# Kernel tuning notes

Hardware: AMD Instinct MI355X
Metric: run time of the kernel (lower is better)

Reference implementation:

```python
import jax, jax.numpy as jnp
import numpy as np

B, T, D, U = 128, 256, 256, 1024


def setup_inputs() -> dict:
    key = jax.random.key(0)
    ks = jax.random.split(key, 5)
    features = jax.random.normal(ks[0], (B, T, D), dtype=jnp.float32)
    # irregular positive time deltas in (0, 1)
    time_steps = jax.random.uniform(ks[1], (B, T), dtype=jnp.float32)
    scale_x = 1.0 / np.sqrt(D)
    scale_h = 1.0 / np.sqrt(U)
    Wx = jax.random.normal(ks[2], (D, 2 * U), dtype=jnp.float32) * scale_x
    Wh = jax.random.normal(ks[3], (U, 2 * U), dtype=jnp.float32) * scale_h
    b = jnp.zeros((2 * U,), dtype=jnp.float32)
    w_tau = jax.random.uniform(ks[4], (U,), dtype=jnp.float32)
    h0 = jnp.zeros((B, U), dtype=jnp.float32)
    return {"features": features, "time_steps": time_steps, "Wx": Wx,
            "Wh": Wh, "b": b, "w_tau": w_tau, "h0": h0}


def reference(features, time_steps, Wx, Wh, b, w_tau, h0):
    """IrregularRNN with exact closed-form LTC cell, return_sequences=True.

    Per step: f = sigmoid(pre_f), A = tanh(pre_a),
              h' = (h - A) * exp(-dt * (softplus(w_tau) + f)) + A
    """
    tau = jax.nn.softplus(w_tau)  # [U]

    def step(h, xt):
        x_t, dt_t = xt                      # [B,D], [B]
        pre = x_t @ Wx + h @ Wh + b         # [B,2U]
        f = jax.nn.sigmoid(pre[:, :U])
        a = jnp.tanh(pre[:, U:])
        decay = jnp.exp(-dt_t[:, None] * (tau + f))
        h_new = (h - a) * decay + a
        return h_new, h_new

    xs = (jnp.swapaxes(features, 0, 1), jnp.swapaxes(time_steps, 0, 1))
    _, ys = jax.lax.scan(step, h0, xs)      # ys: [T,B,U]
    return jnp.swapaxes(ys, 0, 1)           # [B,T,U]
```

## Files before the change

### kernel.cpp

```cpp
#include <hip/hip_runtime.h>

typedef _Float16 v8h  __attribute__((ext_vector_type(8)));
typedef _Float16 v4h  __attribute__((ext_vector_type(4)));
typedef float    v4f  __attribute__((ext_vector_type(4)));
typedef unsigned int u32x4 __attribute__((ext_vector_type(4)));

#define BATCH   128
#define TSTEPS  256
#define DFEAT   256
#define UDIM    1024
#define NCOL    2048
#define ASTRIDE 1288


__global__ __launch_bounds__(1024)
void ltc_rnn_kernel(const float* __restrict__ features,
                    const float* __restrict__ tsteps,
                    const float* __restrict__ Wx,
                    const float* __restrict__ Wh,
                    const float* __restrict__ bias,
                    const float* __restrict__ wtau,
                    const float* __restrict__ h0,
                    float* __restrict__ out,
                    unsigned* __restrict__ flags,
                    _Float16* __restrict__ hbufs)
{
  __shared__ _Float16 Alds[16 * ASTRIDE];
  __shared__ float    Plds[16 * 64 * 4];
  __shared__ _Float16 Hout[16][32];
  __shared__ float    dtlds[2][16];

  const int tid  = threadIdx.x;
  const int w    = tid >> 6;
  const int lane = tid & 63;
  const int n    = lane & 15;
  const int q    = lane >> 4;
  const int cg   = w & 3;
  const int ks   = w >> 2;
  const int g    = blockIdx.x & 7;
  const int cb   = blockIdx.x >> 3;
  const int u0   = cb * 32;

  const int gcol = (n < 8) ? (u0 + cg * 8 + n) : (UDIM + u0 + cg * 8 + (n - 8));
  v8h bfr[10];
  #pragma unroll
  for (int c = 0; c < 10; ++c) {
    #pragma unroll
    for (int j = 0; j < 8; ++j) {
      const int k = ks * 320 + c * 32 + q * 8 + j;
      const float wv = (k < DFEAT) ? Wx[(size_t)k * NCOL + gcol]
                                   : Wh[(size_t)(k - DFEAT) * NCOL + gcol];
      bfr[c][j] = (_Float16)wv;
    }
  }

  const float bias_own = bias[gcol];
  const int   u_lane   = u0 + cg * 8 + (n & 7);
  const float tau      = logf(1.0f + __expf(wtau[u_lane]));

  float h_reg[4];
  #pragma unroll
  for (int i = 0; i < 4; ++i)
    h_reg[i] = h0[(size_t)(g * 16 + q * 4 + i) * UDIM + u_lane];

  if (tid < 16) dtlds[0][tid] = tsteps[(size_t)(g * 16 + tid) * TSTEPS + 0];
  {
    const int r = tid >> 6, k4 = tid & 63;
    v4f x4 = *(const v4f*)(features + (size_t)(g * 16 + r) * (TSTEPS * DFEAT) + k4 * 4);
    v4h xh = {(_Float16)x4.x, (_Float16)x4.y, (_Float16)x4.z, (_Float16)x4.w};
    *(v4h*)&Alds[r * ASTRIDE + k4 * 4] = xh;
    #pragma unroll
    for (int jj = 0; jj < 4; ++jj) {
      const int c = tid + jj * 1024, hr = c >> 8, hk4 = c & 255;
      v4f h4 = *(const v4f*)(h0 + (size_t)(g * 16 + hr) * UDIM + hk4 * 4);
      v4h hh = {(_Float16)h4.x, (_Float16)h4.y, (_Float16)h4.z, (_Float16)h4.w};
      *(v4h*)&Alds[hr * ASTRIDE + DFEAT + hk4 * 4] = hh;
    }
  }
  __syncthreads();

  for (int t = 0; t < TSTEPS; ++t) {
    const bool more = (t + 1 < TSTEPS);
    _Float16* hdst = hbufs + ((t + 1) & 1) * (BATCH * UDIM);

    {
      v4f acc = {0.f, 0.f, 0.f, 0.f};
      const _Float16* abase = &Alds[n * ASTRIDE + ks * 320 + q * 8];
      #pragma unroll
      for (int c = 0; c < 10; ++c) {
        v8h a = *(const v8h*)(abase + c * 32);
        acc = __builtin_amdgcn_mfma_f32_16x16x32_f16(a, bfr[c], acc, 0, 0, 0);
      }
      *(v4f*)&Plds[(w * 64 + lane) * 4] = acc;
    }
    __syncthreads();

    float outv[4];
    if (w < 4) {
      v4f p = *(v4f*)&Plds[((0 * 4 + w) * 64 + lane) * 4];
      #pragma unroll
      for (int s = 1; s < 4; ++s) {
        v4f ps = *(v4f*)&Plds[((s * 4 + w) * 64 + lane) * 4];
        p.x += ps.x; p.y += ps.y; p.z += ps.z; p.w += ps.w;
      }
      float pf[4], pa[4];
      #pragma unroll
      for (int i = 0; i < 4; ++i) {
        const float v = p[i] + bias_own;
        const float o = __shfl_xor(v, 8);
        pf[i] = v; pa[i] = o;
      }
      if (n < 8) {
        #pragma unroll
        for (int i = 0; i < 4; ++i) {
          const int   row_l = q * 4 + i;
          const float dt    = dtlds[t & 1][row_l];
          const float f     = 1.0f / (1.0f + __expf(-pf[i]));
          const float av    = 2.0f / (1.0f + __expf(-2.0f * pa[i])) - 1.0f;
          const float decay = __expf(-dt * (tau + f));
          const float hn    = (h_reg[i] - av) * decay + av;
          h_reg[i] = hn;
          outv[i]  = hn;
          Hout[row_l][w * 8 + n] = (_Float16)hn;
        }
      }
    }
    __syncthreads();

    if (w == 0 && more) {
      const int row = lane >> 2, c8 = lane & 3;
      v8h hv = *(v8h*)&Hout[row][c8 * 8];
      _Float16* dp = hdst + (size_t)(g * 16 + row) * UDIM + u0 + c8 * 8;
      asm volatile("global_store_dwordx4 %0, %1, off sc0 sc1\n\t"
                   "s_waitcnt vmcnt(0)"
                   :: "v"(dp), "v"(__builtin_bit_cast(u32x4, hv)) : "memory");
      if (lane == 0) {
        unsigned tg = (unsigned)(t + 1);
        asm volatile("global_store_dword %0, %1, off sc0 sc1"
                     :: "v"(&flags[g * 64 + cb]), "v"(tg) : "memory");
      }
    }

    if (w < 4 && n < 8) {
      #pragma unroll
      for (int i = 0; i < 4; ++i) {
        const int row = g * 16 + q * 4 + i;
        out[(size_t)row * (TSTEPS * UDIM) + (size_t)t * UDIM + u_lane] = outv[i];
      }
    }
    if (more) {
      if (tid < 16) dtlds[(t + 1) & 1][tid] = tsteps[(size_t)(g * 16 + tid) * TSTEPS + t + 1];
      const int r = tid >> 6, k4 = tid & 63;
      v4f x4 = *(const v4f*)(features + (size_t)(g * 16 + r) * (TSTEPS * DFEAT)
                             + (size_t)(t + 1) * DFEAT + k4 * 4);
      v4h xh = {(_Float16)x4.x, (_Float16)x4.y, (_Float16)x4.z, (_Float16)x4.w};
      *(v4h*)&Alds[r * ASTRIDE + k4 * 4] = xh;
    }

    if (w == 0 && more) {
      const unsigned* fp = &flags[g * 64 + (lane & 31)];
      const unsigned  tg = (unsigned)t;
      for (;;) {
        unsigned v;
        asm volatile("global_load_dword %0, %1, off sc0 sc1\n\t"
                     "s_waitcnt vmcnt(0)"
                     : "=v"(v) : "v"(fp) : "memory");
        if (__ballot(v <= tg) == 0ull) break;
      }
    }
    __syncthreads();

    if (more) {
      const _Float16* hsrc = hbufs + ((t + 1) & 1) * (BATCH * UDIM);
      const int c0 = tid, c1 = tid + 1024;
      const _Float16* p0 = hsrc + (size_t)(g * 16 + (c0 >> 7)) * UDIM + (c0 & 127) * 8;
      const _Float16* p1 = hsrc + (size_t)(g * 16 + (c1 >> 7)) * UDIM + (c1 & 127) * 8;
      u32x4 r0, r1;
      asm volatile("global_load_dwordx4 %0, %2, off sc0 sc1\n\t"
                   "global_load_dwordx4 %1, %3, off sc0 sc1\n\t"
                   "s_waitcnt vmcnt(0)"
                   : "=v"(r0), "=v"(r1) : "v"(p0), "v"(p1) : "memory");
      *(v8h*)&Alds[(c0 >> 7) * ASTRIDE + DFEAT + (c0 & 127) * 8] = __builtin_bit_cast(v8h, r0);
      *(v8h*)&Alds[(c1 >> 7) * ASTRIDE + DFEAT + (c1 & 127) * 8] = __builtin_bit_cast(v8h, r1);
      __syncthreads();
    }
  }
}

extern "C" void kernel_launch(void* const* d_in, const int* in_sizes, int n_in,
                              void* d_out, int out_size, void* d_ws, size_t ws_size,
                              hipStream_t stream) {
  const float* features = (const float*)d_in[0];
  const float* tsamp    = (const float*)d_in[1];
  const float* Wx       = (const float*)d_in[2];
  const float* Wh       = (const float*)d_in[3];
  const float* bias     = (const float*)d_in[4];
  const float* wtau     = (const float*)d_in[5];
  const float* h0       = (const float*)d_in[6];
  float*     out    = (float*)d_out;
  unsigned*  flags  = (unsigned*)d_ws;
  _Float16*  hbufs  = (_Float16*)((char*)d_ws + 4096);

  hipMemsetAsync(d_ws, 0, 4096, stream);
  hipLaunchKernelGGL(ltc_rnn_kernel, dim3(256), dim3(1024), 0, stream,
                     features, tsamp, Wx, Wh, bias, wtau, h0, out, flags, hbufs);
}
```

Measured before the change: 1.029 ms.

## Interleave two batch groups per block to hide cross-block flag waits

Each block now handles two batch groups (gA and gB) using the same column slice, so the grid shrinks from 256 to 128 blocks. The two groups' recurrence phases alternate, so while one group waits for the other blocks' hidden-state flags, the other group's step can run. This is meant to hide global synchronization latency behind independent work. The MFMA chain is also split across two accumulators to cut dependency stalls. In exchange the block needs twice the LDS for the A tiles, and each block now serializes two groups' work, so per-step compute on each CU doubles.

```diff
diff --git a/kernel.cpp b/kernel.cpp
--- a/kernel.cpp
+++ b/kernel.cpp
@@ -13,7 +13,7 @@
 #define ASTRIDE 1288
 
 
-__global__ __launch_bounds__(1024)
+__global__ __launch_bounds__(1024, 4)
 void ltc_rnn_kernel(const float* __restrict__ features,
                     const float* __restrict__ tsteps,
                     const float* __restrict__ Wx,
@@ -25,10 +25,12 @@
                     unsigned* __restrict__ flags,
                     _Float16* __restrict__ hbufs)
 {
-  __shared__ _Float16 Alds[16 * ASTRIDE];
+  __shared__ _Float16 AldsA[16 * ASTRIDE];
+  __shared__ _Float16 AldsB[16 * ASTRIDE];
   __shared__ float    Plds[16 * 64 * 4];
   __shared__ _Float16 Hout[16][32];
-  __shared__ float    dtlds[2][16];
+  __shared__ float    dtA[2][16];
+  __shared__ float    dtB[2][16];
 
   const int tid  = threadIdx.x;
   const int w    = tid >> 6;
@@ -37,9 +39,11 @@
   const int q    = lane >> 4;
   const int cg   = w & 3;
   const int ks   = w >> 2;
-  const int g    = blockIdx.x & 7;
-  const int cb   = blockIdx.x >> 3;
+  const int gp   = blockIdx.x & 3;
+  const int cb   = blockIdx.x >> 2;
   const int u0   = cb * 32;
+  const int gA   = gp;
+  const int gB   = gp + 4;
 
   const int gcol = (n < 8) ? (u0 + cg * 8 + n) : (UDIM + u0 + cg * 8 + (n - 8));
   v8h bfr[10];
@@ -58,108 +62,36 @@
   const int   u_lane   = u0 + cg * 8 + (n & 7);
   const float tau      = logf(1.0f + __expf(wtau[u_lane]));
 
-  float h_reg[4];
+  float h_regA[4], h_regB[4];
   #pragma unroll
-  for (int i = 0; i < 4; ++i)
-    h_reg[i] = h0[(size_t)(g * 16 + q * 4 + i) * UDIM + u_lane];
-
-  if (tid < 16) dtlds[0][tid] = tsteps[(size_t)(g * 16 + tid) * TSTEPS + 0];
-  {
+  for (int i = 0; i < 4; ++i) {
+    h_regA[i] = h0[(size_t)(gA * 16 + q * 4 + i) * UDIM + u_lane];
+    h_regB[i] = h0[(size_t)(gB * 16 + q * 4 + i) * UDIM + u_lane];
+  }
+
+  auto prestage = [&](const int g, _Float16* __restrict__ Ald, float (&dtl)[2][16]) {
+    if (tid < 16) dtl[0][tid] = tsteps[(size_t)(g * 16 + tid) * TSTEPS + 0];
     const int r = tid >> 6, k4 = tid & 63;
     v4f x4 = *(const v4f*)(features + (size_t)(g * 16 + r) * (TSTEPS * DFEAT) + k4 * 4);
     v4h xh = {(_Float16)x4.x, (_Float16)x4.y, (_Float16)x4.z, (_Float16)x4.w};
-    *(v4h*)&Alds[r * ASTRIDE + k4 * 4] = xh;
+    *(v4h*)&Ald[r * ASTRIDE + k4 * 4] = xh;
     #pragma unroll
     for (int jj = 0; jj < 4; ++jj) {
       const int c = tid + jj * 1024, hr = c >> 8, hk4 = c & 255;
       v4f h4 = *(const v4f*)(h0 + (size_t)(g * 16 + hr) * UDIM + hk4 * 4);
       v4h hh = {(_Float16)h4.x, (_Float16)h4.y, (_Float16)h4.z, (_Float16)h4.w};
-      *(v4h*)&Alds[hr * ASTRIDE + DFEAT + hk4 * 4] = hh;
-    }
-  }
+      *(v4h*)&Ald[hr * ASTRIDE + DFEAT + hk4 * 4] = hh;
+    }
+  };
+  prestage(gA, AldsA, dtA);
+  prestage(gB, AldsB, dtB);
   __syncthreads();
 
-  for (int t = 0; t < TSTEPS; ++t) {
-    const bool more = (t + 1 < TSTEPS);
-    _Float16* hdst = hbufs + ((t + 1) & 1) * (BATCH * UDIM);
-
-    {
-      v4f acc = {0.f, 0.f, 0.f, 0.f};
-      const _Float16* abase = &Alds[n * ASTRIDE + ks * 320 + q * 8];
-      #pragma unroll
-      for (int c = 0; c < 10; ++c) {
-        v8h a = *(const v8h*)(abase + c * 32);
-        acc = __builtin_amdgcn_mfma_f32_16x16x32_f16(a, bfr[c], acc, 0, 0, 0);
-      }
-      *(v4f*)&Plds[(w * 64 + lane) * 4] = acc;
-    }
-    __syncthreads();
-
-    float outv[4];
-    if (w < 4) {
-      v4f p = *(v4f*)&Plds[((0 * 4 + w) * 64 + lane) * 4];
-      #pragma unroll
-      for (int s = 1; s < 4; ++s) {
-        v4f ps = *(v4f*)&Plds[((s * 4 + w) * 64 + lane) * 4];
-        p.x += ps.x; p.y += ps.y; p.z += ps.z; p.w += ps.w;
-      }
-      float pf[4], pa[4];
-      #pragma unroll
-      for (int i = 0; i < 4; ++i) {
-        const float v = p[i] + bias_own;
-        const float o = __shfl_xor(v, 8);
-        pf[i] = v; pa[i] = o;
-      }
-      if (n < 8) {
-        #pragma unroll
-        for (int i = 0; i < 4; ++i) {
-          const int   row_l = q * 4 + i;
-          const float dt    = dtlds[t & 1][row_l];
-          const float f     = 1.0f / (1.0f + __expf(-pf[i]));
-          const float av    = 2.0f / (1.0f + __expf(-2.0f * pa[i])) - 1.0f;
-          const float decay = __expf(-dt * (tau + f));
-          const float hn    = (h_reg[i] - av) * decay + av;
-          h_reg[i] = hn;
-          outv[i]  = hn;
-          Hout[row_l][w * 8 + n] = (_Float16)hn;
-        }
-      }
-    }
-    __syncthreads();
-
-    if (w == 0 && more) {
-      const int row = lane >> 2, c8 = lane & 3;
-      v8h hv = *(v8h*)&Hout[row][c8 * 8];
-      _Float16* dp = hdst + (size_t)(g * 16 + row) * UDIM + u0 + c8 * 8;
-      asm volatile("global_store_dwordx4 %0, %1, off sc0 sc1\n\t"
-                   "s_waitcnt vmcnt(0)"
-                   :: "v"(dp), "v"(__builtin_bit_cast(u32x4, hv)) : "memory");
-      if (lane == 0) {
-        unsigned tg = (unsigned)(t + 1);
-        asm volatile("global_store_dword %0, %1, off sc0 sc1"
-                     :: "v"(&flags[g * 64 + cb]), "v"(tg) : "memory");
-      }
-    }
-
-    if (w < 4 && n < 8) {
-      #pragma unroll
-      for (int i = 0; i < 4; ++i) {
-        const int row = g * 16 + q * 4 + i;
-        out[(size_t)row * (TSTEPS * UDIM) + (size_t)t * UDIM + u_lane] = outv[i];
-      }
-    }
-    if (more) {
-      if (tid < 16) dtlds[(t + 1) & 1][tid] = tsteps[(size_t)(g * 16 + tid) * TSTEPS + t + 1];
-      const int r = tid >> 6, k4 = tid & 63;
-      v4f x4 = *(const v4f*)(features + (size_t)(g * 16 + r) * (TSTEPS * DFEAT)
-                             + (size_t)(t + 1) * DFEAT + k4 * 4);
-      v4h xh = {(_Float16)x4.x, (_Float16)x4.y, (_Float16)x4.z, (_Float16)x4.w};
-      *(v4h*)&Alds[r * ASTRIDE + k4 * 4] = xh;
-    }
-
-    if (w == 0 && more) {
+  auto phase = [&](const int g, _Float16* __restrict__ Ald,
+                   float (&hreg)[4], float (&dtl)[2][16], const int t) {
+    if (t > 0) {
       const unsigned* fp = &flags[g * 64 + (lane & 31)];
-      const unsigned  tg = (unsigned)t;
+      const unsigned  tg = (unsigned)(t - 1);
       for (;;) {
         unsigned v;
         asm volatile("global_load_dword %0, %1, off sc0 sc1\n\t"
@@ -167,11 +99,7 @@
                      : "=v"(v) : "v"(fp) : "memory");
         if (__ballot(v <= tg) == 0ull) break;
       }
-    }
-    __syncthreads();
-
-    if (more) {
-      const _Float16* hsrc = hbufs + ((t + 1) & 1) * (BATCH * UDIM);
+      const _Float16* hsrc = hbufs + ((size_t)(t & 1)) * (BATCH * UDIM);
       const int c0 = tid, c1 = tid + 1024;
       const _Float16* p0 = hsrc + (size_t)(g * 16 + (c0 >> 7)) * UDIM + (c0 & 127) * 8;
       const _Float16* p1 = hsrc + (size_t)(g * 16 + (c1 >> 7)) * UDIM + (c1 & 127) * 8;
@@ -180,10 +108,96 @@
                    "global_load_dwordx4 %1, %3, off sc0 sc1\n\t"
                    "s_waitcnt vmcnt(0)"
                    : "=v"(r0), "=v"(r1) : "v"(p0), "v"(p1) : "memory");
-      *(v8h*)&Alds[(c0 >> 7) * ASTRIDE + DFEAT + (c0 & 127) * 8] = __builtin_bit_cast(v8h, r0);
-      *(v8h*)&Alds[(c1 >> 7) * ASTRIDE + DFEAT + (c1 & 127) * 8] = __builtin_bit_cast(v8h, r1);
-      __syncthreads();
-    }
+      *(v8h*)&Ald[(c0 >> 7) * ASTRIDE + DFEAT + (c0 & 127) * 8] = __builtin_bit_cast(v8h, r0);
+      *(v8h*)&Ald[(c1 >> 7) * ASTRIDE + DFEAT + (c1 & 127) * 8] = __builtin_bit_cast(v8h, r1);
+    }
+    __syncthreads();
+
+    {
+      v4f acc0 = {0.f, 0.f, 0.f, 0.f};
+      v4f acc1 = {0.f, 0.f, 0.f, 0.f};
+      const _Float16* abase = &Ald[n * ASTRIDE + ks * 320 + q * 8];
+      #pragma unroll
+      for (int c = 0; c < 10; c += 2) {
+        v8h a0 = *(const v8h*)(abase + c * 32);
+        v8h a1 = *(const v8h*)(abase + (c + 1) * 32);
+        acc0 = __builtin_amdgcn_mfma_f32_16x16x32_f16(a0, bfr[c],     acc0, 0, 0, 0);
+        acc1 = __builtin_amdgcn_mfma_f32_16x16x32_f16(a1, bfr[c + 1], acc1, 0, 0, 0);
+      }
+      v4f acc = acc0 + acc1;
+      *(v4f*)&Plds[(w * 64 + lane) * 4] = acc;
+    }
+    __syncthreads();
+
+    float outv[4];
+    if (w < 4) {
+      v4f p = *(v4f*)&Plds[((0 * 4 + w) * 64 + lane) * 4];
+      #pragma unroll
+      for (int s = 1; s < 4; ++s) {
+        v4f ps = *(v4f*)&Plds[((s * 4 + w) * 64 + lane) * 4];
+        p.x += ps.x; p.y += ps.y; p.z += ps.z; p.w += ps.w;
+      }
+      float pf[4], pa[4];
+      #pragma unroll
+      for (int i = 0; i < 4; ++i) {
+        const float v = p[i] + bias_own;
+        const float o = __shfl_xor(v, 8);
+        pf[i] = v; pa[i] = o;
+      }
+      if (n < 8) {
+        #pragma unroll
+        for (int i = 0; i < 4; ++i) {
+          const int   row_l = q * 4 + i;
+          const float dt    = dtl[t & 1][row_l];
+          const float f     = 1.0f / (1.0f + __expf(-pf[i]));
+          const float av    = 2.0f / (1.0f + __expf(-2.0f * pa[i])) - 1.0f;
+          const float decay = __expf(-dt * (tau + f));
+          const float hn    = (hreg[i] - av) * decay + av;
+          hreg[i] = hn;
+          outv[i] = hn;
+          Hout[row_l][w * 8 + n] = (_Float16)hn;
+        }
+      }
+    }
+    __syncthreads();
+
+    const bool more = (t + 1 < TSTEPS);
+
+    if (w == 0 && more) {
+      const int row = lane >> 2, c8 = lane & 3;
+      v8h hv = *(v8h*)&Hout[row][c8 * 8];
+      _Float16* dp = hbufs + ((size_t)((t + 1) & 1)) * (BATCH * UDIM)
+                   + (size_t)(g * 16 + row) * UDIM + u0 + c8 * 8;
+      asm volatile("global_store_dwordx4 %0, %1, off sc0 sc1\n\t"
+                   "s_waitcnt vmcnt(0)"
+                   :: "v"(dp), "v"(__builtin_bit_cast(u32x4, hv)) : "memory");
+      if (lane == 0) {
+        unsigned tg = (unsigned)(t + 1);
+        asm volatile("global_store_dword %0, %1, off sc0 sc1"
+                     :: "v"(&flags[g * 64 + cb]), "v"(tg) : "memory");
+      }
+    }
+
+    if (w < 4 && n < 8) {
+      #pragma unroll
+      for (int i = 0; i < 4; ++i) {
+        const int row = g * 16 + q * 4 + i;
+        out[(size_t)row * (TSTEPS * UDIM) + (size_t)t * UDIM + u_lane] = outv[i];
+      }
+    }
+    if (more) {
+      if (tid < 16) dtl[(t + 1) & 1][tid] = tsteps[(size_t)(g * 16 + tid) * TSTEPS + t + 1];
+      const int r = tid >> 6, k4 = tid & 63;
+      v4f x4 = *(const v4f*)(features + (size_t)(g * 16 + r) * (TSTEPS * DFEAT)
+                             + (size_t)(t + 1) * DFEAT + k4 * 4);
+      v4h xh = {(_Float16)x4.x, (_Float16)x4.y, (_Float16)x4.z, (_Float16)x4.w};
+      *(v4h*)&Ald[r * ASTRIDE + k4 * 4] = xh;
+    }
+  };
+
+  for (int t = 0; t < TSTEPS; ++t) {
+    phase(gA, AldsA, h_regA, dtA, t);
+    phase(gB, AldsB, h_regB, dtB, t);
   }
 }
 
@@ -202,6 +216,6 @@
   _Float16*  hbufs  = (_Float16*)((char*)d_ws + 4096);
 
   hipMemsetAsync(d_ws, 0, 4096, stream);
-  hipLaunchKernelGGL(ltc_rnn_kernel, dim3(256), dim3(1024), 0, stream,
+  hipLaunchKernelGGL(ltc_rnn_kernel, dim3(128), dim3(1024), 0, stream,
                      features, tsamp, Wx, Wh, bias, wtau, h0, out, flags, hbufs);
 }
```

New measurement: 1.626 ms. 57.9% more time.
